# Kernel tuning notes

Measured on AMD Instinct MI355X. Metric: run time of the kernel, lower is better.

Reference implementation:

```python
import jax, jax.numpy as jnp
import numpy as np

N = 50000          # nodes
E = 800000         # edges (no self loops; self loops added in reference)
D = 128            # in_channels == out_channels (required by index_add into x)
HEADS = 1
NEG_SLOPE = 0.2
NUM_LABELS = 7


def setup_inputs() -> dict:
    key = jax.random.key(0)
    k0, k1, k2, k3, k4, k5 = jax.random.split(key, 6)
    x = jax.random.normal(k0, (N, D), dtype=jnp.float32)
    # edges guaranteed self-loop-free (remove_self_loops is then a no-op)
    src = jax.random.randint(k1, (E,), 0, N, dtype=jnp.int32)
    off = jax.random.randint(k2, (E,), 1, N, dtype=jnp.int32)
    dst = (src + off) % N
    edge_index = jnp.stack([src, dst])  # [2, E]
    node_label = jax.random.randint(k3, (N,), 0, 8, dtype=jnp.int32)  # 0 = inactive, 1..7 active
    glorot = float(np.sqrt(6.0 / (D + D)))
    weight_id = jax.random.uniform(k4, (NUM_LABELS, D, D), jnp.float32, -glorot, glorot)
    ga = float(np.sqrt(6.0 / (HEADS * 2 * D + 1)))
    att = jax.random.uniform(k5, (1, HEADS, 2 * D), jnp.float32, -ga, ga)
    return {"x": x, "edge_index": edge_index, "node_label": node_label,
            "weight_id": weight_id, "att": att}


def reference(x, edge_index, node_label, weight_id, att):
    n, d = x.shape
    # --- per-label identity transform: ox = x + W_{label-1} x for labels 1..7 ---
    y = jnp.einsum('nd,kdo->nko', x, weight_id)           # [N, 7, D]
    valid = (node_label >= 1) & (node_label <= NUM_LABELS)
    idx = jnp.clip(node_label - 1, 0, NUM_LABELS - 1)
    delta = jnp.take_along_axis(y, idx[:, None, None], axis=1)[:, 0]  # [N, D]
    ox = x + jnp.where(valid[:, None], delta, jnp.zeros_like(delta))
    # --- add self loops (input has none) ---
    loops = jnp.arange(n, dtype=edge_index.dtype)
    src = jnp.concatenate([edge_index[0], loops])
    dst = jnp.concatenate([edge_index[1], loops])
    # --- GAT message: gather, attention score, edge softmax over dst ---
    x_j = ox[src].reshape(-1, HEADS, d)                   # [Et, 1, D]
    x_i = ox[dst].reshape(-1, HEADS, d)
    alpha = (x_i * att[:, :, :d]).sum(-1) + (x_j * att[:, :, d:]).sum(-1)  # [Et, 1]
    alpha = jax.nn.leaky_relu(alpha, NEG_SLOPE)
    amax = jax.ops.segment_max(alpha, dst, num_segments=n)  # every node has a self loop
    alpha = jnp.exp(alpha - amax[dst])
    denom = jax.ops.segment_sum(alpha, dst, num_segments=n)
    alpha = alpha / (denom[dst] + 1e-16)
    # dropout p=0 (eval) -> no-op
    msg = (x_j * alpha[:, :, None]).reshape(-1, HEADS * d)  # concat=True, heads=1
    out = jax.ops.segment_sum(msg, dst, num_segments=n)     # [N, D]; bias=False
    return out
```

## Files before the change

kernel.cpp:

```cpp
#include <hip/hip_runtime.h>
#include <math.h>

#define N_NODES 50000
#define N_EDGES 800000
#define DIM 128
#define DEG_CAP 48
#define BINS ((N_NODES + 255) / 256)
#define BIN_CAP 8192
#define EA_CHUNK 3125
#define BA_BLOCKS ((N_EDGES + EA_CHUNK - 1) / EA_CHUNK)

#define LB_BLOCKS ((N_NODES + 255) / 256)
#define WT_BLOCKS ((7 * DIM * DIM + 255) / 256)
#define K1_GRID (BA_BLOCKS + LB_BLOCKS + WT_BLOCKS)

#define TR_BLOCKS 1568
#define K2_GRID (BINS + TR_BLOCKS)

typedef __attribute__((ext_vector_type(8))) short short8;
typedef __attribute__((ext_vector_type(4))) float floatx4;

__device__ __forceinline__ unsigned short f2bf(float f) {
    unsigned int u = __float_as_uint(f);
    unsigned int r = (u + 0x7fff + ((u >> 16) & 1)) >> 16;
    return (unsigned short)r;
}
__device__ __forceinline__ float bf2f_lo(unsigned int v) { return __uint_as_float(v << 16); }
__device__ __forceinline__ float bf2f_hi(unsigned int v) { return __uint_as_float(v & 0xffff0000u); }

__global__ __launch_bounds__(256) void build_kernel(
        const int* __restrict__ src, const int* __restrict__ dst,
        const int* __restrict__ label, const float* __restrict__ W,
        unsigned short* __restrict__ Wt,
        int* __restrict__ bin_cur, unsigned int* __restrict__ binned,
        int* __restrict__ lab_cnt, int* __restrict__ node_list) {
    int t = threadIdx.x;
    int blk = blockIdx.x;

    if (blk < BA_BLOCKS) {
        __shared__ int hist[BINS], base_s[BINS], rank[BINS];
        for (int i = t; i < BINS; i += 256) { hist[i] = 0; rank[i] = 0; }
        __syncthreads();
        int e0 = blk * EA_CHUNK;
        int e1 = e0 + EA_CHUNK; if (e1 > N_EDGES) e1 = N_EDGES;
        for (int e = e0 + t; e < e1; e += 256) atomicAdd(&hist[dst[e] >> 8], 1);
        __syncthreads();
        for (int i = t; i < BINS; i += 256)
            base_s[i] = (hist[i] > 0) ? atomicAdd(&bin_cur[i], hist[i]) : 0;
        __syncthreads();
        for (int e = e0 + t; e < e1; e += 256) {
            int d = dst[e];
            int b = d >> 8;
            int r = atomicAdd(&rank[b], 1);
            int slot = base_s[b] + r;
            if (slot < BIN_CAP)
                binned[(size_t)b * BIN_CAP + slot] = (unsigned int)(src[e] | ((d & 255) << 16));
        }
    } else if (blk < BA_BLOCKS + LB_BLOCKS) {
        __shared__ int lcnt[8], lbase[8], lrank[8];
        int i = (blk - BA_BLOCKS) * 256 + t;
        if (t < 8) { lcnt[t] = 0; lrank[t] = 0; }
        __syncthreads();
        int b = -1;
        if (i < N_NODES) {
            int lab = label[i];
            b = (lab >= 1 && lab <= 7) ? (lab - 1) : 7;
            atomicAdd(&lcnt[b], 1);
        }
        __syncthreads();
        if (t < 8) lbase[t] = (lcnt[t] > 0) ? atomicAdd(&lab_cnt[t], lcnt[t]) : 0;
        __syncthreads();
        if (i < N_NODES) {
            int r = atomicAdd(&lrank[b], 1);
            node_list[(size_t)b * N_NODES + lbase[b] + r] = i;
        }
    } else {
        int j = (blk - BA_BLOCKS - LB_BLOCKS) * 256 + t;
        if (j < 7 * DIM * DIM) {
            int b = j >> 14;
            int d = (j >> 7) & 127;
            int c = j & 127;
            Wt[((size_t)b * DIM + c) * DIM + d] = f2bf(W[j]);
        }
    }
}

__global__ __launch_bounds__(256) void phase2_kernel(
        const float* __restrict__ x, const float* __restrict__ att,
        const int* __restrict__ lab_cnt, const int* __restrict__ node_list,
        const unsigned short* __restrict__ Wt,
        const int* __restrict__ bin_cur, const unsigned int* __restrict__ binned,
        unsigned short* __restrict__ oxh, float* __restrict__ ai, float* __restrict__ aj,
        int* __restrict__ cnt, unsigned short* __restrict__ bucket) {
    int t = threadIdx.x;
    int blk = blockIdx.x;

    if (blk < BINS) {
        __shared__ unsigned short rows[256][DEG_CAP];
        __shared__ int lcnt[256];
        int b = blk;
        int m = bin_cur[b]; if (m > BIN_CAP) m = BIN_CAP;
        const unsigned int* bp = binned + (size_t)b * BIN_CAP;

        lcnt[t] = 0;
        __syncthreads();
        for (int i = t; i < m; i += 256) {
            unsigned int v = bp[i];
            int ln = (v >> 16) & 255;
            int p = atomicAdd(&lcnt[ln], 1);
            if (p < DEG_CAP) rows[ln][p] = (unsigned short)(v & 0xFFFF);
        }
        __syncthreads();
        int n = b * 256 + t;
        if (n < N_NODES) {
            int deg = lcnt[t];
            if (deg > DEG_CAP) deg = DEG_CAP;
            cnt[n] = deg;
        }
        uint4* gdst = (uint4*)(bucket + (size_t)b * 256 * DEG_CAP);
        const uint4* lsrc = (const uint4*)rows;
        #pragma unroll
        for (int k = 0; k < (256 * DEG_CAP * 2 / 16) / 256; k++)
            gdst[t + k * 256] = lsrc[t + k * 256];
    } else {
        int wv = t >> 6;
        int lane = t & 63;
        int gw = (blk - BINS) * 4 + wv;
        int tile = gw >> 1;
        int half = gw & 1;

        int b = 0, base = 0, tcnt = 0;
        for (; b < 8; b++) {
            int c = lab_cnt[b];
            int nt = (c + 15) >> 4;
            if (tile < nt) { base = b * N_NODES + tile * 16; tcnt = c - tile * 16; break; }
            tile -= nt;
        }
        if (b == 8) return;
        if (tcnt > 16) tcnt = 16;

        int m = lane & 15;
        int quad = lane >> 4;

        floatx4 acc[4];
        #pragma unroll
        for (int nt = 0; nt < 4; nt++) acc[nt] = (floatx4){0.f, 0.f, 0.f, 0.f};

        if (b < 7) {
            int mm = (m < tcnt) ? m : 0;
            int nodeA = node_list[base + mm];
            const float* xrow = x + (size_t)nodeA * DIM;
            short8 afrag[4];
            #pragma unroll
            for (int kk = 0; kk < 4; kk++) {
                float4 f0 = *(const float4*)(xrow + kk * 32 + quad * 8);
                float4 f1 = *(const float4*)(xrow + kk * 32 + quad * 8 + 4);
                short8 a;
                a[0] = (short)f2bf(f0.x); a[1] = (short)f2bf(f0.y);
                a[2] = (short)f2bf(f0.z); a[3] = (short)f2bf(f0.w);
                a[4] = (short)f2bf(f1.x); a[5] = (short)f2bf(f1.y);
                a[6] = (short)f2bf(f1.z); a[7] = (short)f2bf(f1.w);
                afrag[kk] = a;
            }

            const unsigned short* WtB = Wt + (size_t)b * DIM * DIM;
            #pragma unroll
            for (int kk = 0; kk < 4; kk++) {
                #pragma unroll
                for (int nt = 0; nt < 4; nt++) {
                    short8 bfrag = *(const short8*)(WtB + (size_t)(half * 64 + nt * 16 + m) * DIM + kk * 32 + quad * 8);
                    acc[nt] = __builtin_amdgcn_mfma_f32_16x16x32_bf16(afrag[kk], bfrag, acc[nt], 0, 0, 0);
                }
            }
        }

        int nodes[4];
        #pragma unroll
        for (int r = 0; r < 4; r++) {
            int rw = quad * 4 + r;
            nodes[r] = node_list[base + ((rw < tcnt) ? rw : 0)];
        }
        float pi[4] = {0.f, 0.f, 0.f, 0.f};
        float pj[4] = {0.f, 0.f, 0.f, 0.f};
        #pragma unroll
        for (int nt = 0; nt < 4; nt++) {
            int c = half * 64 + nt * 16 + m;
            float a1 = att[c];
            float a2 = att[DIM + c];
            #pragma unroll
            for (int r = 0; r < 4; r++) {
                int rw = quad * 4 + r;
                if (rw < tcnt) {
                    float xv = x[(size_t)nodes[r] * DIM + c];
                    float v = (b < 7) ? (acc[nt][r] + xv) : xv;
                    oxh[(size_t)nodes[r] * DIM + c] = f2bf(v);
                    pi[r] += v * a1;
                    pj[r] += v * a2;
                }
            }
        }
        #pragma unroll
        for (int r = 0; r < 4; r++) {
            #pragma unroll
            for (int off = 1; off < 16; off <<= 1) {
                pi[r] += __shfl_xor(pi[r], off, 64);
                pj[r] += __shfl_xor(pj[r], off, 64);
            }
            int rw = quad * 4 + r;
            if (m == 0 && rw < tcnt) {
                atomicAdd(&ai[nodes[r]], pi[r]);
                atomicAdd(&aj[nodes[r]], pj[r]);
            }
        }
    }
}

__global__ __launch_bounds__(256) void gather7_kernel(
        const int* __restrict__ cnt, const unsigned short* __restrict__ bucket,
        const float* __restrict__ ai, const float* __restrict__ aj,
        const uint4* __restrict__ tab,
        float* __restrict__ out) {
    __shared__ float wls[4][64];
    __shared__ int   sls[4][64];
    int wv = threadIdx.x >> 6;
    int lane = threadIdx.x & 63;
    int n = blockIdx.x * 4 + wv;
    int deg = cnt[n];
    if (deg > DEG_CAP) deg = DEG_CAP;
    const unsigned short* row = bucket + (size_t)n * DEG_CAP;
    float ain = ai[n];

    float a = -INFINITY;
    int s = n;
    if (lane < deg) {
        s = row[lane];
        a = ain + aj[s];
        a = (a > 0.0f) ? a : 0.2f * a;
    } else if (lane == deg) {
        a = ain + aj[n];
        a = (a > 0.0f) ? a : 0.2f * a;
    }
    float mx = a;
    #pragma unroll
    for (int off = 32; off > 0; off >>= 1) mx = fmaxf(mx, __shfl_xor(mx, off, 64));
    float w = expf(a - mx);
    float ssum = w;
    #pragma unroll
    for (int off = 32; off > 0; off >>= 1) ssum += __shfl_xor(ssum, off, 64);
    float wn = w / (ssum + 1e-16f);

    wls[wv][lane] = wn;
    sls[wv][lane] = s;
    __syncthreads();

    const float* wp = wls[wv];
    const int*   sp = sls[wv];
    float wsf = wp[deg];

    int g = lane >> 4;
    int cl = lane & 15;
    float ac0 = 0.f, ac1 = 0.f, ac2 = 0.f, ac3 = 0.f;
    float ac4 = 0.f, ac5 = 0.f, ac6 = 0.f, ac7 = 0.f;

    if (g == 0) {
        uint4 v = tab[(size_t)n * 16 + cl];
        ac0 += wsf * bf2f_lo(v.x); ac1 += wsf * bf2f_hi(v.x);
        ac2 += wsf * bf2f_lo(v.y); ac3 += wsf * bf2f_hi(v.y);
        ac4 += wsf * bf2f_lo(v.z); ac5 += wsf * bf2f_hi(v.z);
        ac6 += wsf * bf2f_lo(v.w); ac7 += wsf * bf2f_hi(v.w);
    }

    int niter = (deg + 3) >> 2;
    int k = 0;
    for (; k + 2 <= niter; k += 2) {
        int i0 = g + 4 * k;
        int i1 = i0 + 4;
        float w0 = wp[i0]; int s0 = sp[i0];
        float w1 = wp[i1]; int s1 = sp[i1];
        if (i0 >= deg) w0 = 0.0f;
        if (i1 >= deg) w1 = 0.0f;
        uint4 v0 = tab[(size_t)s0 * 16 + cl];
        uint4 v1 = tab[(size_t)s1 * 16 + cl];
        ac0 += w0 * bf2f_lo(v0.x); ac1 += w0 * bf2f_hi(v0.x);
        ac2 += w0 * bf2f_lo(v0.y); ac3 += w0 * bf2f_hi(v0.y);
        ac4 += w0 * bf2f_lo(v0.z); ac5 += w0 * bf2f_hi(v0.z);
        ac6 += w0 * bf2f_lo(v0.w); ac7 += w0 * bf2f_hi(v0.w);
        ac0 += w1 * bf2f_lo(v1.x); ac1 += w1 * bf2f_hi(v1.x);
        ac2 += w1 * bf2f_lo(v1.y); ac3 += w1 * bf2f_hi(v1.y);
        ac4 += w1 * bf2f_lo(v1.z); ac5 += w1 * bf2f_hi(v1.z);
        ac6 += w1 * bf2f_lo(v1.w); ac7 += w1 * bf2f_hi(v1.w);
    }
    if (k < niter) {
        int i0 = g + 4 * k;
        float w0 = (i0 < deg) ? wp[i0] : 0.0f;
        int s0 = sp[i0];
        uint4 v0 = tab[(size_t)s0 * 16 + cl];
        ac0 += w0 * bf2f_lo(v0.x); ac1 += w0 * bf2f_hi(v0.x);
        ac2 += w0 * bf2f_lo(v0.y); ac3 += w0 * bf2f_hi(v0.y);
        ac4 += w0 * bf2f_lo(v0.z); ac5 += w0 * bf2f_hi(v0.z);
        ac6 += w0 * bf2f_lo(v0.w); ac7 += w0 * bf2f_hi(v0.w);
    }

    #pragma unroll
    for (int off = 16; off < 64; off <<= 1) {
        ac0 += __shfl_xor(ac0, off, 64); ac1 += __shfl_xor(ac1, off, 64);
        ac2 += __shfl_xor(ac2, off, 64); ac3 += __shfl_xor(ac3, off, 64);
        ac4 += __shfl_xor(ac4, off, 64); ac5 += __shfl_xor(ac5, off, 64);
        ac6 += __shfl_xor(ac6, off, 64); ac7 += __shfl_xor(ac7, off, 64);
    }
    if (g == 0) {
        float* op = out + (size_t)n * DIM + cl * 8;
        float4 o0; o0.x = ac0; o0.y = ac1; o0.z = ac2; o0.w = ac3;
        float4 o1; o1.x = ac4; o1.y = ac5; o1.z = ac6; o1.w = ac7;
        *(float4*)op = o0;
        *(float4*)(op + 4) = o1;
    }
}

extern "C" void kernel_launch(void* const* d_in, const int* in_sizes, int n_in,
                              void* d_out, int out_size, void* d_ws, size_t ws_size,
                              hipStream_t stream) {
    const float* x     = (const float*)d_in[0];
    const int*   ei    = (const int*)d_in[1];
    const int*   label = (const int*)d_in[2];
    const float* W     = (const float*)d_in[3];
    const float* att   = (const float*)d_in[4];
    float* out = (float*)d_out;

    const int* src = ei;
    const int* dst = ei + N_EDGES;

    char* w = (char*)d_ws;
    unsigned short* oxh    = (unsigned short*)w; w += sizeof(unsigned short) * (size_t)N_NODES * DIM;
    unsigned short* Wt     = (unsigned short*)w; w += sizeof(unsigned short) * 7 * DIM * DIM;
    unsigned short* bucket = (unsigned short*)w; w += sizeof(unsigned short) * (size_t)BINS * 256 * DEG_CAP;
    unsigned int*   binned = (unsigned int*)w;   w += sizeof(unsigned int) * (size_t)BINS * BIN_CAP;
    int*   cnt       = (int*)w;    w += sizeof(int) * N_NODES;
    int*   node_list = (int*)w;    w += sizeof(int) * (size_t)8 * N_NODES;
    float* ai        = (float*)w;  w += sizeof(float) * N_NODES;
    float* aj        = (float*)w;  w += sizeof(float) * N_NODES;
    int*   lab_cnt   = (int*)w;    w += sizeof(int) * 8;
    int*   bin_cur   = (int*)w;    w += sizeof(int) * BINS;

    hipMemsetAsync(ai, 0, sizeof(float) * 2 * N_NODES + sizeof(int) * (8 + BINS), stream);

    build_kernel<<<K1_GRID, 256, 0, stream>>>(src, dst, label, W,
                                              Wt, bin_cur, binned, lab_cnt, node_list);

    phase2_kernel<<<K2_GRID, 256, 0, stream>>>(x, att, lab_cnt, node_list, Wt,
                                               bin_cur, binned, oxh, ai, aj, cnt, bucket);

    gather7_kernel<<<(N_NODES + 3) / 4, 256, 0, stream>>>(cnt, bucket, ai, aj,
                                                          (const uint4*)oxh, out);
}
```

Before: 169.0 us.

## Stage x tile in LDS per block, reduce attention scores without atomics, unroll gather

Phase2 now gives each block one 16-row tile and splits the 128 output columns across its four waves. The x rows are staged once in shared memory, so the A fragments and the residual reads come from LDS instead of repeated global loads. The ai/aj dot products are reduced across waves in shared memory and written directly, which removes the float atomics and shrinks the memset. The gather loop is unrolled to four outstanding row loads per iteration, at the cost of more registers.

```diff
diff --git a/kernel.cpp b/kernel.cpp
--- a/kernel.cpp
+++ b/kernel.cpp
@@ -14,8 +14,10 @@
 #define WT_BLOCKS ((7 * DIM * DIM + 255) / 256)
 #define K1_GRID (BA_BLOCKS + LB_BLOCKS + WT_BLOCKS)
 
-#define TR_BLOCKS 1568
-#define K2_GRID (BINS + TR_BLOCKS)
+#define TR_TILES 3133
+#define K2_GRID (BINS + TR_TILES)
+
+#define XS_STRIDE 132
 
 typedef __attribute__((ext_vector_type(8))) short short8;
 typedef __attribute__((ext_vector_type(4))) float floatx4;
@@ -92,12 +94,13 @@
         const int* __restrict__ bin_cur, const unsigned int* __restrict__ binned,
         unsigned short* __restrict__ oxh, float* __restrict__ ai, float* __restrict__ aj,
         int* __restrict__ cnt, unsigned short* __restrict__ bucket) {
+    __shared__ __align__(16) char smem[25600];
     int t = threadIdx.x;
     int blk = blockIdx.x;
 
     if (blk < BINS) {
-        __shared__ unsigned short rows[256][DEG_CAP];
-        __shared__ int lcnt[256];
+        unsigned short (*rows)[DEG_CAP] = (unsigned short (*)[DEG_CAP])smem;
+        int* lcnt = (int*)(smem + 24576);
         int b = blk;
         int m = bin_cur[b]; if (m > BIN_CAP) m = BIN_CAP;
         const unsigned int* bp = binned + (size_t)b * BIN_CAP;
@@ -123,12 +126,7 @@
         for (int k = 0; k < (256 * DEG_CAP * 2 / 16) / 256; k++)
             gdst[t + k * 256] = lsrc[t + k * 256];
     } else {
-        int wv = t >> 6;
-        int lane = t & 63;
-        int gw = (blk - BINS) * 4 + wv;
-        int tile = gw >> 1;
-        int half = gw & 1;
-
+        int tile = blk - BINS;
         int b = 0, base = 0, tcnt = 0;
         for (; b < 8; b++) {
             int c = lab_cnt[b];
@@ -139,37 +137,50 @@
         if (b == 8) return;
         if (tcnt > 16) tcnt = 16;
 
+        float* xs  = (float*)smem;
+        float* red = (float*)(smem + 16 * XS_STRIDE * 4);
+
+        {
+            const float4* x4 = (const float4*)x;
+            int j = t;
+            #pragma unroll
+            for (int k = 0; k < 2; k++, j += 256) {
+                int row = j >> 5;
+                int c4  = j & 31;
+                int node = node_list[base + ((row < tcnt) ? row : 0)];
+                float4 v = x4[(size_t)node * 32 + c4];
+                *(float4*)(xs + row * XS_STRIDE + c4 * 4) = v;
+            }
+        }
+        __syncthreads();
+
+        int wv = t >> 6;
+        int lane = t & 63;
         int m = lane & 15;
         int quad = lane >> 4;
 
-        floatx4 acc[4];
-        #pragma unroll
-        for (int nt = 0; nt < 4; nt++) acc[nt] = (floatx4){0.f, 0.f, 0.f, 0.f};
+        floatx4 acc[2];
+        acc[0] = (floatx4){0.f, 0.f, 0.f, 0.f};
+        acc[1] = (floatx4){0.f, 0.f, 0.f, 0.f};
 
         if (b < 7) {
-            int mm = (m < tcnt) ? m : 0;
-            int nodeA = node_list[base + mm];
-            const float* xrow = x + (size_t)nodeA * DIM;
             short8 afrag[4];
             #pragma unroll
             for (int kk = 0; kk < 4; kk++) {
-                float4 f0 = *(const float4*)(xrow + kk * 32 + quad * 8);
-                float4 f1 = *(const float4*)(xrow + kk * 32 + quad * 8 + 4);
+                const float* xp = xs + m * XS_STRIDE + kk * 32 + quad * 8;
                 short8 a;
-                a[0] = (short)f2bf(f0.x); a[1] = (short)f2bf(f0.y);
-                a[2] = (short)f2bf(f0.z); a[3] = (short)f2bf(f0.w);
-                a[4] = (short)f2bf(f1.x); a[5] = (short)f2bf(f1.y);
-                a[6] = (short)f2bf(f1.z); a[7] = (short)f2bf(f1.w);
+                #pragma unroll
+                for (int e = 0; e < 8; e++) a[e] = (short)f2bf(xp[e]);
                 afrag[kk] = a;
             }
-
             const unsigned short* WtB = Wt + (size_t)b * DIM * DIM;
             #pragma unroll
             for (int kk = 0; kk < 4; kk++) {
                 #pragma unroll
-                for (int nt = 0; nt < 4; nt++) {
-                    short8 bfrag = *(const short8*)(WtB + (size_t)(half * 64 + nt * 16 + m) * DIM + kk * 32 + quad * 8);
-                    acc[nt] = __builtin_amdgcn_mfma_f32_16x16x32_bf16(afrag[kk], bfrag, acc[nt], 0, 0, 0);
+                for (int nl = 0; nl < 2; nl++) {
+                    int c = wv * 32 + nl * 16 + m;
+                    short8 bfrag = *(const short8*)(WtB + (size_t)c * DIM + kk * 32 + quad * 8);
+                    acc[nl] = __builtin_amdgcn_mfma_f32_16x16x32_bf16(afrag[kk], bfrag, acc[nl], 0, 0, 0);
                 }
             }
         }
@@ -183,16 +194,16 @@
         float pi[4] = {0.f, 0.f, 0.f, 0.f};
         float pj[4] = {0.f, 0.f, 0.f, 0.f};
         #pragma unroll
-        for (int nt = 0; nt < 4; nt++) {
-            int c = half * 64 + nt * 16 + m;
+        for (int nl = 0; nl < 2; nl++) {
+            int c = wv * 32 + nl * 16 + m;
             float a1 = att[c];
             float a2 = att[DIM + c];
             #pragma unroll
             for (int r = 0; r < 4; r++) {
                 int rw = quad * 4 + r;
                 if (rw < tcnt) {
-                    float xv = x[(size_t)nodes[r] * DIM + c];
-                    float v = (b < 7) ? (acc[nt][r] + xv) : xv;
+                    float xv = xs[rw * XS_STRIDE + c];
+                    float v = (b < 7) ? (acc[nl][r] + xv) : xv;
                     oxh[(size_t)nodes[r] * DIM + c] = f2bf(v);
                     pi[r] += v * a1;
                     pj[r] += v * a2;
@@ -206,16 +217,30 @@
                 pi[r] += __shfl_xor(pi[r], off, 64);
                 pj[r] += __shfl_xor(pj[r], off, 64);
             }
-            int rw = quad * 4 + r;
-            if (m == 0 && rw < tcnt) {
-                atomicAdd(&ai[nodes[r]], pi[r]);
-                atomicAdd(&aj[nodes[r]], pj[r]);
-            }
-        }
-    }
-}
-
-__global__ __launch_bounds__(256) void gather7_kernel(
+        }
+        if (m == 0) {
+            #pragma unroll
+            for (int r = 0; r < 4; r++) {
+                red[wv * 32 + quad * 4 + r]      = pi[r];
+                red[wv * 32 + 16 + quad * 4 + r] = pj[r];
+            }
+        }
+        __syncthreads();
+        if (t < 16 && t < tcnt) {
+            int node = node_list[base + t];
+            float si = 0.f, sj = 0.f;
+            #pragma unroll
+            for (int w2 = 0; w2 < 4; w2++) {
+                si += red[w2 * 32 + t];
+                sj += red[w2 * 32 + 16 + t];
+            }
+            ai[node] = si;
+            aj[node] = sj;
+        }
+    }
+}
+
+__global__ __launch_bounds__(256) void gather8_kernel(
         const int* __restrict__ cnt, const unsigned short* __restrict__ bucket,
         const float* __restrict__ ai, const float* __restrict__ aj,
         const uint4* __restrict__ tab,
@@ -272,15 +297,20 @@
 
     int niter = (deg + 3) >> 2;
     int k = 0;
-    for (; k + 2 <= niter; k += 2) {
-        int i0 = g + 4 * k;
-        int i1 = i0 + 4;
+    for (; k + 4 <= niter; k += 4) {
+        int i0 = g + 4 * k, i1 = i0 + 4, i2 = i0 + 8, i3 = i0 + 12;
         float w0 = wp[i0]; int s0 = sp[i0];
         float w1 = wp[i1]; int s1 = sp[i1];
+        float w2 = wp[i2]; int s2 = sp[i2];
+        float w3 = wp[i3]; int s3 = sp[i3];
         if (i0 >= deg) w0 = 0.0f;
         if (i1 >= deg) w1 = 0.0f;
+        if (i2 >= deg) w2 = 0.0f;
+        if (i3 >= deg) w3 = 0.0f;
         uint4 v0 = tab[(size_t)s0 * 16 + cl];
         uint4 v1 = tab[(size_t)s1 * 16 + cl];
+        uint4 v2 = tab[(size_t)s2 * 16 + cl];
+        uint4 v3 = tab[(size_t)s3 * 16 + cl];
         ac0 += w0 * bf2f_lo(v0.x); ac1 += w0 * bf2f_hi(v0.x);
         ac2 += w0 * bf2f_lo(v0.y); ac3 += w0 * bf2f_hi(v0.y);
         ac4 += w0 * bf2f_lo(v0.z); ac5 += w0 * bf2f_hi(v0.z);
@@ -289,8 +319,16 @@
         ac2 += w1 * bf2f_lo(v1.y); ac3 += w1 * bf2f_hi(v1.y);
         ac4 += w1 * bf2f_lo(v1.z); ac5 += w1 * bf2f_hi(v1.z);
         ac6 += w1 * bf2f_lo(v1.w); ac7 += w1 * bf2f_hi(v1.w);
-    }
-    if (k < niter) {
+        ac0 += w2 * bf2f_lo(v2.x); ac1 += w2 * bf2f_hi(v2.x);
+        ac2 += w2 * bf2f_lo(v2.y); ac3 += w2 * bf2f_hi(v2.y);
+        ac4 += w2 * bf2f_lo(v2.z); ac5 += w2 * bf2f_hi(v2.z);
+        ac6 += w2 * bf2f_lo(v2.w); ac7 += w2 * bf2f_hi(v2.w);
+        ac0 += w3 * bf2f_lo(v3.x); ac1 += w3 * bf2f_hi(v3.x);
+        ac2 += w3 * bf2f_lo(v3.y); ac3 += w3 * bf2f_hi(v3.y);
+        ac4 += w3 * bf2f_lo(v3.z); ac5 += w3 * bf2f_hi(v3.z);
+        ac6 += w3 * bf2f_lo(v3.w); ac7 += w3 * bf2f_hi(v3.w);
+    }
+    for (; k < niter; k++) {
         int i0 = g + 4 * k;
         float w0 = (i0 < deg) ? wp[i0] : 0.0f;
         int s0 = sp[i0];
@@ -342,7 +380,7 @@
     int*   lab_cnt   = (int*)w;    w += sizeof(int) * 8;
     int*   bin_cur   = (int*)w;    w += sizeof(int) * BINS;
 
-    hipMemsetAsync(ai, 0, sizeof(float) * 2 * N_NODES + sizeof(int) * (8 + BINS), stream);
+    hipMemsetAsync(lab_cnt, 0, sizeof(int) * (8 + BINS), stream);
 
     build_kernel<<<K1_GRID, 256, 0, stream>>>(src, dst, label, W,
                                               Wt, bin_cur, binned, lab_cnt, node_list);
@@ -350,6 +388,6 @@
     phase2_kernel<<<K2_GRID, 256, 0, stream>>>(x, att, lab_cnt, node_list, Wt,
                                                bin_cur, binned, oxh, ai, aj, cnt, bucket);
 
-    gather7_kernel<<<(N_NODES + 3) / 4, 256, 0, stream>>>(cnt, bucket, ai, aj,
+    gather8_kernel<<<(N_NODES + 3) / 4, 256, 0, stream>>>(cnt, bucket, ai, aj,
                                                           (const uint4*)oxh, out);
 }
```

After: 156.5 us. 7.4% less time.
